# Optimization experiments

Measured on AMD Instinct MI355X. Metric: run time of the kernel, lower is better.

The kernel has to match this reference:

```python
import jax, jax.numpy as jnp
import numpy as np

H_DIM = 768
NUM_HEADS = 12
HEAD_DIM = H_DIM // NUM_HEADS
ROPE_BASE = 10000.0


def rope_cos_sin(seq_len, dim):
    inv_freq = 1.0 / (ROPE_BASE ** (jnp.arange(0, dim, 2, dtype=jnp.float32) / dim))
    t = jnp.arange(seq_len, dtype=jnp.float32)
    freqs = jnp.outer(t, inv_freq)              # [seq, dim/2]
    emb = jnp.concatenate([freqs, freqs], axis=-1)  # [seq, dim]
    return jnp.cos(emb), jnp.sin(emb)


def rotate_half(x):
    x1, x2 = jnp.split(x, 2, axis=-1)
    return jnp.concatenate([-x2, x1], axis=-1)


def setup_inputs() -> dict:
    key = jax.random.key(0)
    ks = jax.random.split(key, 9)
    s = 1.0 / np.sqrt(H_DIM)
    inp = {
        'x': jax.random.normal(ks[0], (2, 8, 1024, H_DIM), dtype=jnp.float32),
        'Wq': jax.random.normal(ks[1], (H_DIM, H_DIM), dtype=jnp.float32) * s,
        'bq': jnp.zeros((H_DIM,), dtype=jnp.float32),
        'Wk': jax.random.normal(ks[2], (H_DIM, H_DIM), dtype=jnp.float32) * s,
        'bk': jnp.zeros((H_DIM,), dtype=jnp.float32),
        'Wv': jax.random.normal(ks[3], (H_DIM, H_DIM), dtype=jnp.float32) * s,
        'bv': jnp.zeros((H_DIM,), dtype=jnp.float32),
        'Wo': jax.random.normal(ks[4], (H_DIM, H_DIM), dtype=jnp.float32) * s,
        'bo': jnp.zeros((H_DIM,), dtype=jnp.float32),
        'mask': jnp.ones((2, 8, 1, 1, 1024), dtype=jnp.int32),
    }
    return inp


def reference(x, Wq, bq, Wk, bk, Wv, bv, Wo, bo, mask):
    b, r, s, d = x.shape
    H, D = NUM_HEADS, HEAD_DIM

    def proj(W, bvec):
        # [b,r,s,d] -> [b,r,H,s,D]
        y = x @ W + bvec
        return y.reshape(b, r, s, H, D).transpose(0, 1, 3, 2, 4)

    q = proj(Wq, bq)
    k = proj(Wk, bk)
    v = proj(Wv, bv)

    cos, sin = rope_cos_sin(s, D)   # [s, D]
    cos = cos[None, None, None]     # broadcast over b,r,H
    sin = sin[None, None, None]
    q = q * cos + rotate_half(q) * sin
    k = k * cos + rotate_half(k) * sin

    scores = jnp.einsum('brhqd,brhkd->brhqk', q, k) / jnp.sqrt(jnp.float32(D))
    scores = jnp.where(mask == 0, -jnp.inf, scores)
    probs = jax.nn.softmax(scores, axis=-1)  # dropout is identity in eval
    out = jnp.einsum('brhqk,brhkd->brhqd', probs, v)
    out = out.transpose(0, 1, 3, 2, 4).reshape(b, r, s, d)
    return out @ Wo + bo
```

## Files before the change

kernel.cpp:

```cpp
#include <hip/hip_runtime.h>


#define M_TOT 16384
#define DM    768
#define NH    12
#define HD    64
#define SEQ   1024

typedef __attribute__((ext_vector_type(8))) __bf16 bf16x8;
typedef __attribute__((ext_vector_type(4))) __bf16 bf16x4;
typedef __attribute__((ext_vector_type(4))) short s16x4;
typedef __attribute__((ext_vector_type(4))) float  f32x4;

static __device__ __forceinline__ unsigned short f2b(float f) {
  unsigned u = __builtin_bit_cast(unsigned, f);
  u += 0x7FFFu + ((u >> 16) & 1u);
  return (unsigned short)(u >> 16);
}
static __device__ __forceinline__ float b2f(unsigned short s) {
  unsigned u = ((unsigned)s) << 16;
  return __builtin_bit_cast(float, u);
}
static __device__ __forceinline__ unsigned cvt_pk_bf16(float lo, float hi) {
  unsigned d;
  asm("v_cvt_pk_bf16_f32 %0, %1, %2" : "=v"(d) : "v"(lo), "v"(hi));
  return d;
}

static __device__ __forceinline__ f32x4 mfma16(uint2 a, uint2 b, f32x4 c) {
#if __has_builtin(__builtin_amdgcn_mfma_f32_16x16x16_bf16)
  union U { uint2 u; bf16x4 v; } A, B;
  A.u = a; B.u = b;
  return __builtin_amdgcn_mfma_f32_16x16x16_bf16(A.v, B.v, c, 0, 0, 0);
#else
  union U { uint2 u; s16x4 v; } A, B;
  A.u = a; B.u = b;
  return __builtin_amdgcn_mfma_f32_16x16x16bf16_1k(A.v, B.v, c, 0, 0, 0);
#endif
}

static __device__ __forceinline__ void gl_lds16(const void* g, void* l) {
  __builtin_amdgcn_global_load_lds(
      (const __attribute__((address_space(1))) unsigned*)g,
      (__attribute__((address_space(3))) unsigned*)l, 16, 0, 0);
}

static __device__ __forceinline__ int swz_src(int c) {
  return ((c >> 3) << 6) + (((c & 7) ^ ((c >> 3) & 7)) << 3);
}
static __device__ __forceinline__ int swz_rd(int row, int col16) {
  return (row << 6) + ((col16 ^ (row & 7)) << 3);
}

__global__ void cvt_x(const float* __restrict__ x, unsigned short* __restrict__ xb) {
  const int n4 = M_TOT * DM / 4;
  for (int i = blockIdx.x * blockDim.x + threadIdx.x; i < n4; i += gridDim.x * blockDim.x) {
    float4 v = ((const float4*)x)[i];
    ushort4 o;
    o.x = f2b(v.x); o.y = f2b(v.y); o.z = f2b(v.z); o.w = f2b(v.w);
    ((ushort4*)xb)[i] = o;
  }
}

__global__ void prep(const float* __restrict__ Wq, const float* __restrict__ Wk,
                     const float* __restrict__ Wv, const float* __restrict__ Wo,
                     unsigned short* __restrict__ Wt,
                     float* __restrict__ cosT, float* __restrict__ sinT,
                     const float* __restrict__ bq, const float* __restrict__ bk,
                     const float* __restrict__ bv, float* __restrict__ bcat) {
  __shared__ float T[64][65];
  const int bid = blockIdx.x;
  const int t = threadIdx.x;
  if (bid < 576) {
    const int wsel = bid / 144, r144 = bid % 144;
    const int k0 = (r144 % 12) * 64, n0 = (r144 / 12) * 64;
    const float* W = wsel == 0 ? Wq : wsel == 1 ? Wk : wsel == 2 ? Wv : Wo;
#pragma unroll
    for (int p = 0; p < 16; ++p) {
      int e = p * 256 + t, r = e >> 6, c = e & 63;
      T[r][c] = W[(size_t)(k0 + r) * DM + n0 + c];
    }
    __syncthreads();
    unsigned short* dst = Wt + (size_t)wsel * DM * DM;
#pragma unroll
    for (int p = 0; p < 16; ++p) {
      int e = p * 256 + t, r = e >> 6, c = e & 63;
      dst[(size_t)(n0 + r) * DM + k0 + c] = f2b(T[c][r]);
    }
  } else if (bid < 704) {
    int i = (bid - 576) * 256 + t;
    int s = i >> 5, j = i & 31;
    float inv = powf(10000.0f, -(float)j * (1.0f / 32.0f));
    float ang = (float)s * inv;
    cosT[i] = cosf(ang);
    sinT[i] = sinf(ang);
  } else {
    int i = (bid - 704) * 256 + t;
    if (i < 3 * DM)
      bcat[i] = i < DM ? bq[i] : (i < 2 * DM ? bk[i - DM] : bv[i - 2 * DM]);
  }
}

static __device__ __forceinline__ void gemm_core(const unsigned short* __restrict__ A,
                                                 const unsigned short* __restrict__ Bt,
                                                 int m0, int n0, f32x4 acc[4][4],
                                                 char* smem) {
  unsigned short* As = (unsigned short*)smem;
  unsigned short* Bs = As + 128 * 64;
  const int tid = threadIdx.x, lane = tid & 63, w = tid >> 6;
  const int wr = w >> 1, wc = w & 1;
  const int lr = lane & 15, g4 = lane >> 4;

#pragma unroll
  for (int i = 0; i < 4; ++i)
#pragma unroll
    for (int j = 0; j < 4; ++j) acc[i][j] = (f32x4){0.f, 0.f, 0.f, 0.f};

  auto STAGE = [&](int k0) {
#pragma unroll
    for (int p = 0; p < 4; ++p) {
      int cb = p * 256 + w * 64;
      int c = cb + lane;
      const int ro = c >> 3;
      const int co = ((c & 7) ^ (ro & 7)) << 3;
      gl_lds16(A + (size_t)(m0 + ro) * DM + k0 + co, (char*)As + cb * 16);
      gl_lds16(Bt + (size_t)(n0 + ro) * DM + k0 + co, (char*)Bs + cb * 16);
    }
  };

  STAGE(0);
  __syncthreads();

  for (int kt = 0; kt < DM / 64; ++kt) {
    bf16x8 a[4], b[4];
    {
      const int ch = g4;
#pragma unroll
      for (int i = 0; i < 4; ++i) {
        const int row = wr * 64 + i * 16 + lr;
        a[i] = *(const bf16x8*)&As[(row << 6) + ((ch ^ (row & 7)) << 3)];
      }
#pragma unroll
      for (int j = 0; j < 4; ++j) {
        const int row = wc * 64 + j * 16 + lr;
        b[j] = *(const bf16x8*)&Bs[(row << 6) + ((ch ^ (row & 7)) << 3)];
      }
      __builtin_amdgcn_s_setprio(1);
#pragma unroll
      for (int i = 0; i < 4; ++i)
#pragma unroll
        for (int j = 0; j < 4; ++j)
          acc[i][j] = __builtin_amdgcn_mfma_f32_16x16x32_bf16(a[i], b[j], acc[i][j], 0, 0, 0);
      __builtin_amdgcn_s_setprio(0);
    }
    bf16x8 a1[4], b1[4];
    {
      const int ch = 4 + g4;
#pragma unroll
      for (int i = 0; i < 4; ++i) {
        const int row = wr * 64 + i * 16 + lr;
        a1[i] = *(const bf16x8*)&As[(row << 6) + ((ch ^ (row & 7)) << 3)];
      }
#pragma unroll
      for (int j = 0; j < 4; ++j) {
        const int row = wc * 64 + j * 16 + lr;
        b1[j] = *(const bf16x8*)&Bs[(row << 6) + ((ch ^ (row & 7)) << 3)];
      }
    }
    __syncthreads();
    if (kt + 1 < DM / 64) STAGE((kt + 1) * 64);
    __builtin_amdgcn_s_setprio(1);
#pragma unroll
    for (int i = 0; i < 4; ++i)
#pragma unroll
      for (int j = 0; j < 4; ++j)
        acc[i][j] = __builtin_amdgcn_mfma_f32_16x16x32_bf16(a1[i], b1[j], acc[i][j], 0, 0, 0);
    __builtin_amdgcn_s_setprio(0);
    __syncthreads();
  }
}

__global__ __launch_bounds__(256, 4) void gemm_qkv(
    const unsigned short* __restrict__ xb, const unsigned short* __restrict__ Wt,
    const float* __restrict__ bcat, const float* __restrict__ cosT,
    const float* __restrict__ sinT, unsigned short* __restrict__ Qh,
    unsigned short* __restrict__ Kh, unsigned short* __restrict__ Vt) {
  __shared__ alignas(16) char smem[32768];
  const int id = blockIdx.x;
  const int xcdc = id & 7, rem = id >> 3;
  const int y = rem % 18, xc = rem / 18;
  const int xm = xc * 8 + xcdc;
  const int m0 = xm * 128, n0 = y * 128;
  f32x4 acc[4][4];
  gemm_core(xb, Wt, m0, n0, acc, smem);

  const int tid = threadIdx.x, lane = tid & 63, w = tid >> 6;
  const int wr = w >> 1, wc = w & 1;
  const int lr = lane & 15, g4 = lane >> 4;
  const int zone = y / 6;
  const int wcol0 = n0 - zone * DM + wc * 64;
  const int h = wcol0 >> 6;
  const int br = m0 >> 10;
  const int s_base = (m0 & 1023) + wr * 64;

  if (zone == 2) {
    unsigned short* dstb = Vt + ((size_t)(br * NH + h) * HD) * SEQ;
#pragma unroll
    for (int j = 0; j < 4; ++j) {
      const int d = j * 16 + lr;
      const float bv = bcat[n0 + wc * 64 + d];
#pragma unroll
      for (int i = 0; i < 4; ++i) {
        const int s0 = s_base + i * 16 + g4 * 4;
        ushort4 st;
        st.x = f2b(acc[i][j][0] + bv);
        st.y = f2b(acc[i][j][1] + bv);
        st.z = f2b(acc[i][j][2] + bv);
        st.w = f2b(acc[i][j][3] + bv);
        *(ushort4*)&dstb[(size_t)d * SEQ + s0] = st;
      }
    }
  } else {
    const float sc = zone == 0 ? 0.125f * 1.44269504f : 1.0f;
    unsigned short* dstb = (zone ? Kh : Qh) + ((size_t)(br * NH + h) * SEQ) * HD;
    char* Wb = smem + (size_t)w * 8192;
    const int s_q = s_base + lane;
    const int bcol = n0 + wc * 64;

#pragma unroll
    for (int hh = 0; hh < 2; ++hh) {
#pragma unroll
      for (int jj = 0; jj < 2; ++jj) {
        const int jp = hh + jj * 2;
        const float bv = bcat[bcol + jp * 16 + lr];
        const int dslot = jj * 16 + lr;
        const int sub = (dslot & 3) * 4;
        const int ch = dslot >> 2;
#pragma unroll
        for (int i = 0; i < 4; ++i) {
#pragma unroll
          for (int r = 0; r < 4; ++r) {
            const int s_loc = i * 16 + g4 * 4 + r;
            *(float*)(Wb + s_loc * 128 + ((ch ^ (s_loc & 7)) << 4) + sub) =
                (acc[i][jp][r] + bv) * sc;
          }
        }
      }
      unsigned short* drow = dstb + (size_t)s_q * HD + hh * 16;
      const char* Rb = Wb + lane * 128;
      const int lx = lane & 7;
#pragma unroll
      for (int c = 0; c < 4; ++c) {
        f32x4 va = *(const f32x4*)(Rb + ((c ^ lx) << 4));
        f32x4 vb = *(const f32x4*)(Rb + (((c + 4) ^ lx) << 4));
        float4 c4 = *(const float4*)&cosT[s_q * 32 + hh * 16 + c * 4];
        float4 s4 = *(const float4*)&sinT[s_q * 32 + hh * 16 + c * 4];
        uint2 oa, ob;
        oa.x = cvt_pk_bf16(va[0] * c4.x - vb[0] * s4.x, va[1] * c4.y - vb[1] * s4.y);
        oa.y = cvt_pk_bf16(va[2] * c4.z - vb[2] * s4.z, va[3] * c4.w - vb[3] * s4.w);
        ob.x = cvt_pk_bf16(vb[0] * c4.x + va[0] * s4.x, vb[1] * c4.y + va[1] * s4.y);
        ob.y = cvt_pk_bf16(vb[2] * c4.z + va[2] * s4.z, vb[3] * c4.w + va[3] * s4.w);
        *(uint2*)(drow + c * 4)      = oa;
        *(uint2*)(drow + 32 + c * 4) = ob;
      }
    }
  }
}

__global__ __launch_bounds__(256, 4) void gemm_o(const unsigned short* __restrict__ attnb,
                                                 const unsigned short* __restrict__ WtO,
                                                 const float* __restrict__ bo,
                                                 float* __restrict__ out) {
  __shared__ alignas(16) char smem[32768];
  const int id = blockIdx.x;
  const int xcdc = id & 7, rem = id >> 3;
  const int y = rem % 6, xc = rem / 6;
  const int m0 = (xc * 8 + xcdc) * 128, n0 = y * 128;
  f32x4 acc[4][4];
  gemm_core(attnb, WtO, m0, n0, acc, smem);
  const int tid = threadIdx.x, lane = tid & 63, w = tid >> 6;
  const int wr = w >> 1, wc = w & 1;
  const int lr = lane & 15, g4 = lane >> 4;
#pragma unroll
  for (int j = 0; j < 4; ++j) {
    const int col = n0 + wc * 64 + j * 16 + lr;
    const float bv = bo[col];
#pragma unroll
    for (int i = 0; i < 4; ++i) {
      const int rowb = m0 + wr * 64 + i * 16 + g4 * 4;
#pragma unroll
      for (int r = 0; r < 4; ++r)
        out[(size_t)(rowb + r) * DM + col] = acc[i][j][r] + bv;
    }
  }
}

__global__ __launch_bounds__(256) void attn_fwd(const unsigned short* __restrict__ Qh,
                                                const unsigned short* __restrict__ Kh,
                                                const unsigned short* __restrict__ Vt,
                                                const int* __restrict__ mask,
                                                unsigned short* __restrict__ attnb) {
  __shared__ unsigned short Ks[2][64 * 64];
  __shared__ unsigned short Vs[2][64 * 64];
  const int id = blockIdx.x;
  const int xcdc = id & 7, rem = id >> 3;
  const int qt = rem & 15, g = rem >> 4;
  const int brh = g * 8 + xcdc;
  const int br = brh / NH, h = brh - br * NH;
  const int tid = threadIdx.x, lane = tid & 63, w = tid >> 6;
  const int lr = lane & 15, g4 = lane >> 4;

  const unsigned short* Kg = Kh + (size_t)brh * SEQ * HD;
  const unsigned short* Vg = Vt + (size_t)brh * HD * SEQ;
  const int* mrow0 = mask + (size_t)br * SEQ + g4 * 4;

  int4 mi = *(const int4*)&mask[(size_t)br * SEQ + tid * 4];
  const int allLive = __syncthreads_and(mi.x && mi.y && mi.z && mi.w);

#pragma unroll
  for (int p = 0; p < 2; ++p) {
    int cb = p * 256 + w * 64;
    int c = cb + lane;
    gl_lds16(Kg + swz_src(c), (char*)Ks[0] + cb * 16);
    gl_lds16(Vg + (size_t)(c >> 3) * SEQ + (((c & 7) ^ ((c >> 3) & 7)) << 3),
             (char*)Vs[0] + cb * 16);
  }

  const unsigned short* Qg = Qh + ((size_t)brh * SEQ + qt * 64 + w * 16 + lr) * HD;
  bf16x8 qa[2];
  qa[0] = *(const bf16x8*)(Qg + g4 * 8);
  qa[1] = *(const bf16x8*)(Qg + 32 + g4 * 8);

  f32x4 o[4], lacc;
#pragma unroll
  for (int j = 0; j < 4; ++j) o[j] = (f32x4){0.f, 0.f, 0.f, 0.f};
  lacc = (f32x4){0.f, 0.f, 0.f, 0.f};
  const uint2 ones = {0x3F803F80u, 0x3F803F80u};

  __syncthreads();

  unsigned short* KsC = Ks[0];
  unsigned short* VsC = Vs[0];
  unsigned short* KsN = Ks[1];
  unsigned short* VsN = Vs[1];

  for (int kb = 0; kb < SEQ / 64; ++kb) {
    if (kb + 1 < SEQ / 64) {
#pragma unroll
      for (int p = 0; p < 2; ++p) {
        int cb = p * 256 + w * 64;
        int c = cb + lane;
        gl_lds16(Kg + (size_t)(kb + 1) * 64 * HD + swz_src(c), (char*)KsN + cb * 16);
        gl_lds16(Vg + (size_t)(c >> 3) * SEQ + (kb + 1) * 64 +
                     (((c & 7) ^ ((c >> 3) & 7)) << 3),
                 (char*)VsN + cb * 16);
      }
    }

    f32x4 s4[4];
#pragma unroll
    for (int j = 0; j < 4; ++j) s4[j] = (f32x4){0.f, 0.f, 0.f, 0.f};
    __builtin_amdgcn_s_setprio(1);
#pragma unroll
    for (int kk = 0; kk < 2; ++kk) {
#pragma unroll
      for (int j = 0; j < 4; ++j) {
        bf16x8 kf = *(const bf16x8*)&KsC[swz_rd(j * 16 + lr, kk * 4 + g4)];
        s4[j] = __builtin_amdgcn_mfma_f32_16x16x32_bf16(kf, qa[kk], s4[j], 0, 0, 0);
      }
    }
    __builtin_amdgcn_s_setprio(0);

    if (!allLive) {
      const int* mr = mrow0 + kb * 64;
#pragma unroll
      for (int j = 0; j < 4; ++j) {
        int4 mq = *(const int4*)&mr[j * 16];
        s4[j][0] += mq.x ? 0.f : -3e38f;
        s4[j][1] += mq.y ? 0.f : -3e38f;
        s4[j][2] += mq.z ? 0.f : -3e38f;
        s4[j][3] += mq.w ? 0.f : -3e38f;
      }
    }

    uint2 wb[4];
#pragma unroll
    for (int j = 0; j < 4; ++j) {
      wb[j].x = cvt_pk_bf16(exp2f(s4[j][0]), exp2f(s4[j][1]));
      wb[j].y = cvt_pk_bf16(exp2f(s4[j][2]), exp2f(s4[j][3]));
    }

    __builtin_amdgcn_s_setprio(1);
#pragma unroll
    for (int j = 0; j < 4; ++j) lacc = mfma16(ones, wb[j], lacc);
#pragma unroll
    for (int jj = 0; jj < 4; ++jj) {
      const int row = jj * 16 + lr;
#pragma unroll
      for (int j = 0; j < 4; ++j) {
        const int c8 = j * 4 + g4;
        uint2 av = *(const uint2*)&VsC[(row << 6) + ((((c8 >> 1) ^ (lr & 7))) << 3) +
                                       ((c8 & 1) << 2)];
        o[jj] = mfma16(av, wb[j], o[jj]);
      }
    }
    __builtin_amdgcn_s_setprio(0);

    __syncthreads();
    unsigned short* t;
    t = KsC; KsC = KsN; KsN = t;
    t = VsC; VsC = VsN; VsN = t;
  }

  float l = lacc[0];
  float inv = l > 0.f ? 1.0f / l : 0.f;
  unsigned short* dst =
      attnb + ((size_t)(br * SEQ + qt * 64 + w * 16 + lr)) * DM + h * HD;
#pragma unroll
  for (int j = 0; j < 4; ++j) {
    ushort4 st;
    st.x = f2b(o[j][0] * inv);
    st.y = f2b(o[j][1] * inv);
    st.z = f2b(o[j][2] * inv);
    st.w = f2b(o[j][3] * inv);
    *(ushort4*)&dst[j * 16 + g4 * 4] = st;
  }
}

extern "C" void kernel_launch(void* const* d_in, const int* in_sizes, int n_in,
                              void* d_out, int out_size, void* d_ws, size_t ws_size,
                              hipStream_t stream) {
  const float* x  = (const float*)d_in[0];
  const float* Wq = (const float*)d_in[1];
  const float* bq = (const float*)d_in[2];
  const float* Wk = (const float*)d_in[3];
  const float* bk = (const float*)d_in[4];
  const float* Wv = (const float*)d_in[5];
  const float* bv = (const float*)d_in[6];
  const float* Wo = (const float*)d_in[7];
  const float* bo = (const float*)d_in[8];
  const int* mask = (const int*)d_in[9];
  float* out = (float*)d_out;

  const size_t OFF_XB   = 0;
  const size_t OFF_WT   = 25165824;
  const size_t OFF_COS  = 29884416;
  const size_t OFF_SIN  = 30015488;
  const size_t OFF_BC   = 30146560;
  const size_t OFF_ATT  = 30158848;
  const size_t OFF_QH   = 55324672;
  const size_t OFF_KH   = 80490496;
  const size_t OFF_VT   = 105656320;
  const size_t REQUIRED = 130822144;
  if (ws_size < REQUIRED) return;

  char* w = (char*)d_ws;
  unsigned short* xb   = (unsigned short*)(w + OFF_XB);
  unsigned short* Wt   = (unsigned short*)(w + OFF_WT);
  float* cosT          = (float*)(w + OFF_COS);
  float* sinT          = (float*)(w + OFF_SIN);
  float* bcat          = (float*)(w + OFF_BC);
  unsigned short* attnb = (unsigned short*)(w + OFF_ATT);
  unsigned short* Qh   = (unsigned short*)(w + OFF_QH);
  unsigned short* Kh   = (unsigned short*)(w + OFF_KH);
  unsigned short* Vt   = (unsigned short*)(w + OFF_VT);

  cvt_x<<<2048, 256, 0, stream>>>(x, xb);
  prep<<<713, 256, 0, stream>>>(Wq, Wk, Wv, Wo, Wt, cosT, sinT, bq, bk, bv, bcat);
  gemm_qkv<<<2304, 256, 0, stream>>>(xb, Wt, bcat, cosT, sinT, Qh, Kh, Vt);
  attn_fwd<<<3072, 256, 0, stream>>>(Qh, Kh, Vt, mask, attnb);
  gemm_o<<<768, 256, 0, stream>>>(attnb, Wt + (size_t)3 * DM * DM, bo, out);
}
```

Measured before the change: 236.1 us.

## Process two query tiles per attention block to reuse staged K/V tiles

Each attention workgroup now handles 128 query rows (two 64-row tiles) instead of 64, so every K/V tile loaded into LDS feeds twice as many MFMAs. The grid halves from 3072 to 1536 blocks, cutting global K/V traffic and barrier count per unit of work. The cost is more accumulator registers per thread, which may lower occupancy, and fewer blocks to spread across the CUs.

```diff
diff --git a/kernel.cpp b/kernel.cpp
--- a/kernel.cpp
+++ b/kernel.cpp
@@ -304,7 +304,7 @@
   __shared__ unsigned short Vs[2][64 * 64];
   const int id = blockIdx.x;
   const int xcdc = id & 7, rem = id >> 3;
-  const int qt = rem & 15, g = rem >> 4;
+  const int qp = rem & 7, g = rem >> 3;
   const int brh = g * 8 + xcdc;
   const int br = brh / NH, h = brh - br * NH;
   const int tid = threadIdx.x, lane = tid & 63, w = tid >> 6;
@@ -326,15 +326,22 @@
              (char*)Vs[0] + cb * 16);
   }
 
-  const unsigned short* Qg = Qh + ((size_t)brh * SEQ + qt * 64 + w * 16 + lr) * HD;
-  bf16x8 qa[2];
-  qa[0] = *(const bf16x8*)(Qg + g4 * 8);
-  qa[1] = *(const bf16x8*)(Qg + 32 + g4 * 8);
-
-  f32x4 o[4], lacc;
-#pragma unroll
-  for (int j = 0; j < 4; ++j) o[j] = (f32x4){0.f, 0.f, 0.f, 0.f};
-  lacc = (f32x4){0.f, 0.f, 0.f, 0.f};
+  const unsigned short* Qg0 =
+      Qh + ((size_t)brh * SEQ + qp * 128 + w * 16 + lr) * HD;
+  bf16x8 qa0[2], qa1[2];
+  qa0[0] = *(const bf16x8*)(Qg0 + g4 * 8);
+  qa0[1] = *(const bf16x8*)(Qg0 + 32 + g4 * 8);
+  qa1[0] = *(const bf16x8*)(Qg0 + (size_t)64 * HD + g4 * 8);
+  qa1[1] = *(const bf16x8*)(Qg0 + (size_t)64 * HD + 32 + g4 * 8);
+
+  f32x4 o0[4], o1[4], lacc0, lacc1;
+#pragma unroll
+  for (int j = 0; j < 4; ++j) {
+    o0[j] = (f32x4){0.f, 0.f, 0.f, 0.f};
+    o1[j] = (f32x4){0.f, 0.f, 0.f, 0.f};
+  }
+  lacc0 = (f32x4){0.f, 0.f, 0.f, 0.f};
+  lacc1 = (f32x4){0.f, 0.f, 0.f, 0.f};
   const uint2 ones = {0x3F803F80u, 0x3F803F80u};
 
   __syncthreads();
@@ -357,54 +364,61 @@
       }
     }
 
-    f32x4 s4[4];
-#pragma unroll
-    for (int j = 0; j < 4; ++j) s4[j] = (f32x4){0.f, 0.f, 0.f, 0.f};
-    __builtin_amdgcn_s_setprio(1);
-#pragma unroll
-    for (int kk = 0; kk < 2; ++kk) {
+#pragma unroll
+    for (int qi = 0; qi < 2; ++qi) {
+      const bf16x8* qa = qi ? qa1 : qa0;
+      f32x4* o = qi ? o1 : o0;
+      f32x4& lacc = qi ? lacc1 : lacc0;
+
+      f32x4 s4[4];
+#pragma unroll
+      for (int j = 0; j < 4; ++j) s4[j] = (f32x4){0.f, 0.f, 0.f, 0.f};
+      __builtin_amdgcn_s_setprio(1);
+#pragma unroll
+      for (int kk = 0; kk < 2; ++kk) {
+#pragma unroll
+        for (int j = 0; j < 4; ++j) {
+          bf16x8 kf = *(const bf16x8*)&KsC[swz_rd(j * 16 + lr, kk * 4 + g4)];
+          s4[j] = __builtin_amdgcn_mfma_f32_16x16x32_bf16(kf, qa[kk], s4[j], 0, 0, 0);
+        }
+      }
+      __builtin_amdgcn_s_setprio(0);
+
+      if (!allLive) {
+        const int* mr = mrow0 + kb * 64;
+#pragma unroll
+        for (int j = 0; j < 4; ++j) {
+          int4 mq = *(const int4*)&mr[j * 16];
+          s4[j][0] += mq.x ? 0.f : -3e38f;
+          s4[j][1] += mq.y ? 0.f : -3e38f;
+          s4[j][2] += mq.z ? 0.f : -3e38f;
+          s4[j][3] += mq.w ? 0.f : -3e38f;
+        }
+      }
+
+      uint2 wb[4];
 #pragma unroll
       for (int j = 0; j < 4; ++j) {
-        bf16x8 kf = *(const bf16x8*)&KsC[swz_rd(j * 16 + lr, kk * 4 + g4)];
-        s4[j] = __builtin_amdgcn_mfma_f32_16x16x32_bf16(kf, qa[kk], s4[j], 0, 0, 0);
-      }
-    }
-    __builtin_amdgcn_s_setprio(0);
-
-    if (!allLive) {
-      const int* mr = mrow0 + kb * 64;
-#pragma unroll
-      for (int j = 0; j < 4; ++j) {
-        int4 mq = *(const int4*)&mr[j * 16];
-        s4[j][0] += mq.x ? 0.f : -3e38f;
-        s4[j][1] += mq.y ? 0.f : -3e38f;
-        s4[j][2] += mq.z ? 0.f : -3e38f;
-        s4[j][3] += mq.w ? 0.f : -3e38f;
-      }
-    }
-
-    uint2 wb[4];
-#pragma unroll
-    for (int j = 0; j < 4; ++j) {
-      wb[j].x = cvt_pk_bf16(exp2f(s4[j][0]), exp2f(s4[j][1]));
-      wb[j].y = cvt_pk_bf16(exp2f(s4[j][2]), exp2f(s4[j][3]));
-    }
-
-    __builtin_amdgcn_s_setprio(1);
-#pragma unroll
-    for (int j = 0; j < 4; ++j) lacc = mfma16(ones, wb[j], lacc);
-#pragma unroll
-    for (int jj = 0; jj < 4; ++jj) {
-      const int row = jj * 16 + lr;
-#pragma unroll
-      for (int j = 0; j < 4; ++j) {
-        const int c8 = j * 4 + g4;
-        uint2 av = *(const uint2*)&VsC[(row << 6) + ((((c8 >> 1) ^ (lr & 7))) << 3) +
-                                       ((c8 & 1) << 2)];
-        o[jj] = mfma16(av, wb[j], o[jj]);
-      }
-    }
-    __builtin_amdgcn_s_setprio(0);
+        wb[j].x = cvt_pk_bf16(exp2f(s4[j][0]), exp2f(s4[j][1]));
+        wb[j].y = cvt_pk_bf16(exp2f(s4[j][2]), exp2f(s4[j][3]));
+      }
+
+      __builtin_amdgcn_s_setprio(1);
+#pragma unroll
+      for (int j = 0; j < 4; ++j) lacc = mfma16(ones, wb[j], lacc);
+#pragma unroll
+      for (int jj = 0; jj < 4; ++jj) {
+        const int row = jj * 16 + lr;
+#pragma unroll
+        for (int j = 0; j < 4; ++j) {
+          const int c8 = j * 4 + g4;
+          uint2 av = *(const uint2*)&VsC[(row << 6) + ((((c8 >> 1) ^ (lr & 7))) << 3) +
+                                         ((c8 & 1) << 2)];
+          o[jj] = mfma16(av, wb[j], o[jj]);
+        }
+      }
+      __builtin_amdgcn_s_setprio(0);
+    }
 
     __syncthreads();
     unsigned short* t;
@@ -412,18 +426,22 @@
     t = VsC; VsC = VsN; VsN = t;
   }
 
-  float l = lacc[0];
-  float inv = l > 0.f ? 1.0f / l : 0.f;
-  unsigned short* dst =
-      attnb + ((size_t)(br * SEQ + qt * 64 + w * 16 + lr)) * DM + h * HD;
-#pragma unroll
-  for (int j = 0; j < 4; ++j) {
-    ushort4 st;
-    st.x = f2b(o[j][0] * inv);
-    st.y = f2b(o[j][1] * inv);
-    st.z = f2b(o[j][2] * inv);
-    st.w = f2b(o[j][3] * inv);
-    *(ushort4*)&dst[j * 16 + g4 * 4] = st;
+#pragma unroll
+  for (int qi = 0; qi < 2; ++qi) {
+    f32x4* o = qi ? o1 : o0;
+    float l = qi ? lacc1[0] : lacc0[0];
+    float inv = l > 0.f ? 1.0f / l : 0.f;
+    unsigned short* dst =
+        attnb + ((size_t)(br * SEQ + qp * 128 + qi * 64 + w * 16 + lr)) * DM + h * HD;
+#pragma unroll
+    for (int j = 0; j < 4; ++j) {
+      ushort4 st;
+      st.x = f2b(o[j][0] * inv);
+      st.y = f2b(o[j][1] * inv);
+      st.z = f2b(o[j][2] * inv);
+      st.w = f2b(o[j][3] * inv);
+      *(ushort4*)&dst[j * 16 + g4 * 4] = st;
+    }
   }
 }
 
@@ -468,6 +486,6 @@
   cvt_x<<<2048, 256, 0, stream>>>(x, xb);
   prep<<<713, 256, 0, stream>>>(Wq, Wk, Wv, Wo, Wt, cosT, sinT, bq, bk, bv, bcat);
   gemm_qkv<<<2304, 256, 0, stream>>>(xb, Wt, bcat, cosT, sinT, Qh, Kh, Vt);
-  attn_fwd<<<3072, 256, 0, stream>>>(Qh, Kh, Vt, mask, attnb);
+  attn_fwd<<<1536, 256, 0, stream>>>(Qh, Kh, Vt, mask, attnb);
   gemm_o<<<768, 256, 0, stream>>>(attnb, Wt + (size_t)3 * DM * DM, bo, out);
 }
```

New measurement: 231.0 us (median of 2 runs). -2.2%, faster.
